# Performance work log

Hardware: AMD Instinct MI355X
Metric: run time of the kernel (lower is better)

The kernel has to match this reference:

```python
import jax, jax.numpy as jnp
import numpy as np

N = 10000
E = 160000
NEG_SLOPE = 0.2  # PyG GATConv default leaky_relu slope


def _gat_layer(x, src, dst, W, a_src, a_dst, b):
    """PyG GATConv with concat=True, add_self_loops=False.
    x: [N, Fin], W: [Fin, H*C], a_src/a_dst: [H, C], b: [H*C].
    """
    H, C = a_src.shape
    h = (x @ W).reshape(-1, H, C)                      # [N, H, C]
    al_s = jnp.sum(h * a_src, axis=-1)                 # [N, H]
    al_d = jnp.sum(h * a_dst, axis=-1)                 # [N, H]
    e = jax.nn.leaky_relu(al_s[src] + al_d[dst], NEG_SLOPE)  # [E, H]
    # segment softmax over edges grouped by destination node
    m = jax.ops.segment_max(e, dst, num_segments=N)    # [N, H]
    m = jnp.where(jnp.isfinite(m), m, 0.0)
    ex = jnp.exp(e - m[dst])                           # [E, H]
    den = jax.ops.segment_sum(ex, dst, num_segments=N)  # [N, H]
    alpha = ex / jnp.maximum(den[dst], 1e-16)          # [E, H]
    # scatter-add weighted source features
    out = jax.ops.segment_sum(alpha[:, :, None] * h[src], dst, num_segments=N)  # [N, H, C]
    return out.reshape(-1, H * C) + b


def setup_inputs() -> dict:
    key = jax.random.key(0)
    ks = jax.random.split(key, 16)
    s = 0.05
    return {
        "x": jax.random.normal(ks[0], (N, 300), jnp.float32),
        "edge_index": jax.random.randint(ks[1], (2, E), 0, N, jnp.int32),
        "W1": jax.random.normal(ks[2], (300, 512), jnp.float32) * s,
        "att_src1": jax.random.normal(ks[3], (4, 128), jnp.float32) * s,
        "att_dst1": jax.random.normal(ks[4], (4, 128), jnp.float32) * s,
        "b1": jax.random.normal(ks[5], (512,), jnp.float32) * s,
        "Wl1": jax.random.normal(ks[6], (300, 512), jnp.float32) * s,
        "bl1": jax.random.normal(ks[7], (512,), jnp.float32) * s,
        "W2": jax.random.normal(ks[8], (512, 2048), jnp.float32) * s,
        "att_src2": jax.random.normal(ks[9], (4, 512), jnp.float32) * s,
        "att_dst2": jax.random.normal(ks[10], (4, 512), jnp.float32) * s,
        "b2": jax.random.normal(ks[11], (2048,), jnp.float32) * s,
        "Wl2": jax.random.normal(ks[12], (512, 2048), jnp.float32) * s,
        "bl2": jax.random.normal(ks[13], (2048,), jnp.float32) * s,
    }


def reference(x, edge_index, W1, att_src1, att_dst1, b1, Wl1, bl1,
              W2, att_src2, att_dst2, b2, Wl2, bl2):
    src, dst = edge_index[0], edge_index[1]
    h1 = _gat_layer(x, src, dst, W1, att_src1, att_dst1, b1) + (x @ Wl1 + bl1)
    h1 = jax.nn.relu(h1)
    out = _gat_layer(h1, src, dst, W2, att_src2, att_dst2, b2) + (h1 @ Wl2 + bl2)
    return out
```

## Files before the change

kernel.cpp:

```cpp
#include <hip/hip_runtime.h>
#include <hip/hip_bf16.h>
#include <cstdint>


__device__ __forceinline__ float lrelu(float v) { return v >= 0.f ? v : 0.2f * v; }

__device__ __forceinline__ short f2bf(float x) {
  unsigned u = __float_as_uint(x);
  unsigned r = (u + 0x7fffu + ((u >> 16) & 1u)) >> 16;
  return (short)r;
}
__device__ __forceinline__ float bf2f(short b) {
  return __uint_as_float(((unsigned)(unsigned short)b) << 16);
}

typedef __attribute__((ext_vector_type(8))) short bf16x8;
typedef __attribute__((ext_vector_type(4))) float f32x4;

__device__ __forceinline__ void gload_lds16(const void* g, void* l) {
  auto gp = (const __attribute__((address_space(1))) unsigned int*)(uintptr_t)g;
  auto lp = (__attribute__((address_space(3))) unsigned int*)(uintptr_t)l;
  __builtin_amdgcn_global_load_lds(gp, lp, 16, 0, 0);
}

__global__ void count_edges_k(const int* __restrict__ dstv, int* __restrict__ counts, int E) {
  int e = blockIdx.x * 256 + threadIdx.x;
  if (e < E) atomicAdd(&counts[dstv[e]], 1);
}

__global__ void scan_k(const int* __restrict__ counts, int* __restrict__ rowptr,
                       int* __restrict__ cursor, int n) {
  __shared__ int wsum[16];
  __shared__ int s_base;
  int tid = threadIdx.x, lane = tid & 63, wv = tid >> 6;
  if (tid == 0) s_base = 0;
  __syncthreads();
  for (int base = 0; base < n; base += 1024) {
    int i = base + tid;
    int v = (i < n) ? counts[i] : 0;
    int x = v;
#pragma unroll
    for (int off = 1; off < 64; off <<= 1) {
      int t = __shfl_up(x, off);
      if (lane >= off) x += t;
    }
    if (lane == 63) wsum[wv] = x;
    __syncthreads();
    int woff = 0, tot = 0;
#pragma unroll
    for (int w = 0; w < 16; ++w) {
      int s = wsum[w];
      tot += s;
      if (w < wv) woff += s;
    }
    int b = s_base;
    if (i < n) {
      int excl = b + woff + x - v;
      rowptr[i] = excl;
      cursor[i] = excl;
    }
    __syncthreads();
    if (tid == 0) s_base = b + tot;
  }
  __syncthreads();
  if (tid == 0) rowptr[n] = s_base;
}

__global__ void fill_csr_k(const int* __restrict__ srcv, const int* __restrict__ dstv,
                           int* __restrict__ cursor, int* __restrict__ csr_src, int E) {
  int e = blockIdx.x * 256 + threadIdx.x;
  if (e < E) {
    int p = atomicAdd(&cursor[dstv[e]], 1);
    csr_src[p] = srcv[e];
  }
}

template <bool BIAS>
__global__ __launch_bounds__(256) void gemm_k(
    const float* __restrict__ A, const float* __restrict__ B,
    const float* __restrict__ bias, float* __restrict__ C,
    int M, int N, int K) {
  constexpr int BK = 16;
  __shared__ float As[BK][68];
  __shared__ float Bs[BK][64];
  int tid = threadIdx.x;
  int tx = tid & 15, ty = tid >> 4;
  int m0 = blockIdx.y * 64, n0 = blockIdx.x * 64;
  float acc[4][4] = {};
  int arow = tid >> 2, akq = (tid & 3) * 4;
  int bk = tid >> 4, bnq = (tid & 15) * 4;

  for (int k0 = 0; k0 < K; k0 += BK) {
    float4 av;
    int gm = m0 + arow, gk = k0 + akq;
    if (gm < M && gk + 3 < K) {
      av = *(const float4*)(A + (size_t)gm * K + gk);
    } else {
      av.x = (gm < M && gk + 0 < K) ? A[(size_t)gm * K + gk + 0] : 0.f;
      av.y = (gm < M && gk + 1 < K) ? A[(size_t)gm * K + gk + 1] : 0.f;
      av.z = (gm < M && gk + 2 < K) ? A[(size_t)gm * K + gk + 2] : 0.f;
      av.w = (gm < M && gk + 3 < K) ? A[(size_t)gm * K + gk + 3] : 0.f;
    }
    float4 bv = make_float4(0.f, 0.f, 0.f, 0.f);
    int gbk = k0 + bk;
    if (gbk < K) bv = *(const float4*)(B + (size_t)gbk * N + n0 + bnq);

    As[akq + 0][arow] = av.x;
    As[akq + 1][arow] = av.y;
    As[akq + 2][arow] = av.z;
    As[akq + 3][arow] = av.w;
    *(float4*)&Bs[bk][bnq] = bv;
    __syncthreads();

#pragma unroll
    for (int kk = 0; kk < BK; ++kk) {
      float4 a4 = *(const float4*)&As[kk][ty * 4];
      float4 b4 = *(const float4*)&Bs[kk][tx * 4];
      float a[4] = {a4.x, a4.y, a4.z, a4.w};
      float b[4] = {b4.x, b4.y, b4.z, b4.w};
#pragma unroll
      for (int i = 0; i < 4; ++i)
#pragma unroll
        for (int j = 0; j < 4; ++j) acc[i][j] = fmaf(a[i], b[j], acc[i][j]);
    }
    __syncthreads();
  }

#pragma unroll
  for (int i = 0; i < 4; ++i) {
    int gm = m0 + ty * 4 + i;
    if (gm >= M) continue;
    float4 o;
    float bx = 0.f, by = 0.f, bz = 0.f, bw = 0.f;
    if (BIAS) {
      bx = bias[n0 + tx * 4 + 0];
      by = bias[n0 + tx * 4 + 1];
      bz = bias[n0 + tx * 4 + 2];
      bw = bias[n0 + tx * 4 + 3];
    }
    o.x = acc[i][0] + bx;
    o.y = acc[i][1] + by;
    o.z = acc[i][2] + bz;
    o.w = acc[i][3] + bw;
    *(float4*)(C + (size_t)gm * N + n0 + tx * 4) = o;
  }
}

__global__ void wsplit_t_k(const float* __restrict__ W, short* __restrict__ Wth,
                           short* __restrict__ Wtl, int Nn) {
  int idx = blockIdx.x * 256 + threadIdx.x;
  if (idx >= Nn * 512) return;
  int k = idx & 511;
  int n = idx >> 9;
  float a = W[(size_t)k * Nn + n];
  short h = f2bf(a);
  Wth[idx] = h;
  Wtl[idx] = f2bf(a - bf2f(h));
}

template <bool BIAS>
__global__ __launch_bounds__(256) void gemm_bf16x3_k(
    const short* __restrict__ Ah, const short* __restrict__ Al,
    const short* __restrict__ Bh, const short* __restrict__ Bl,
    const float* __restrict__ bias, float* __restrict__ C,
    int M, int Nn, int K) {
  __shared__ __align__(16) short Ash[128 * 32];
  __shared__ __align__(16) short Asl[128 * 32];
  __shared__ __align__(16) short Bsh[128 * 32];
  __shared__ __align__(16) short Bsl[128 * 32];
  int tid = threadIdx.x, w = tid >> 6, l = tid & 63;
  int m0 = blockIdx.y * 128, n0 = blockIdx.x * 128;
  int wm = (w >> 1) * 64, wn = (w & 1) * 64;

  f32x4 acc[4][4] = {};

  int r_in = l >> 2;
  int kq = (l & 3) * 8;
  int arow_base = m0 + w * 32 + r_in;
  int brow_base = n0 + w * 32 + r_in;
  int lbase = (w * 32) * 32;

  int fr = l & 15, fk = (l >> 4) * 8;

  for (int k0 = 0; k0 < K; k0 += 32) {
    __syncthreads();
#pragma unroll
    for (int i = 0; i < 2; ++i) {
      int am = min(arow_base + i * 16, M - 1);
      int bn = brow_base + i * 16;
      size_t aoff = (size_t)am * K + k0 + kq;
      size_t boff = (size_t)bn * K + k0 + kq;
      int lofs = lbase + i * (16 * 32);
      gload_lds16(Ah + aoff, &Ash[lofs]);
      gload_lds16(Al + aoff, &Asl[lofs]);
      gload_lds16(Bh + boff, &Bsh[lofs]);
      gload_lds16(Bl + boff, &Bsl[lofs]);
    }
    __syncthreads();

    bf16x8 afh[4], afl[4], bfh[4], bfl[4];
#pragma unroll
    for (int t = 0; t < 4; ++t) {
      int ar = wm + t * 16 + fr;
      afh[t] = *(const bf16x8*)&Ash[ar * 32 + fk];
      afl[t] = *(const bf16x8*)&Asl[ar * 32 + fk];
      int br = wn + t * 16 + fr;
      bfh[t] = *(const bf16x8*)&Bsh[br * 32 + fk];
      bfl[t] = *(const bf16x8*)&Bsl[br * 32 + fk];
    }
#pragma unroll
    for (int mi = 0; mi < 4; ++mi)
#pragma unroll
      for (int ni = 0; ni < 4; ++ni) {
        acc[mi][ni] = __builtin_amdgcn_mfma_f32_16x16x32_bf16(afh[mi], bfh[ni], acc[mi][ni], 0, 0, 0);
        acc[mi][ni] = __builtin_amdgcn_mfma_f32_16x16x32_bf16(afh[mi], bfl[ni], acc[mi][ni], 0, 0, 0);
        acc[mi][ni] = __builtin_amdgcn_mfma_f32_16x16x32_bf16(afl[mi], bfh[ni], acc[mi][ni], 0, 0, 0);
      }
  }

  int fq = (l >> 4) * 4;
#pragma unroll
  for (int ni = 0; ni < 4; ++ni) {
    int gc = n0 + wn + ni * 16 + fr;
    float bv = BIAS ? bias[gc] : 0.f;
#pragma unroll
    for (int mi = 0; mi < 4; ++mi) {
      int grb = m0 + wm + mi * 16 + fq;
#pragma unroll
      for (int r = 0; r < 4; ++r) {
        int gr = grb + r;
        if (gr < M) C[(size_t)gr * Nn + gc] = acc[mi][ni][r] + bv;
      }
    }
  }
}

template <int C>
__global__ __launch_bounds__(256) void att_coef_k(
    const float* __restrict__ hfeat, const float* __restrict__ a_src,
    const float* __restrict__ a_dst, float* __restrict__ al_s,
    float* __restrict__ al_d, int n) {
  int wave = threadIdx.x >> 6, lane = threadIdx.x & 63;
  int node = blockIdx.x * 4 + wave;
  if (node >= n) return;
  constexpr int F = 4 * C;
  const float* hrow = hfeat + (size_t)node * F;
  float s[4] = {0, 0, 0, 0}, d[4] = {0, 0, 0, 0};
  for (int f = lane; f < F; f += 64) {
    float hv = hrow[f];
    int h = f / C;
    s[h] = fmaf(hv, a_src[f], s[h]);
    d[h] = fmaf(hv, a_dst[f], d[h]);
  }
#pragma unroll
  for (int off = 32; off; off >>= 1) {
#pragma unroll
    for (int h = 0; h < 4; ++h) {
      s[h] += __shfl_xor(s[h], off);
      d[h] += __shfl_xor(d[h], off);
    }
  }
  if (lane == 0) {
#pragma unroll
    for (int h = 0; h < 4; ++h) {
      al_s[node * 4 + h] = s[h];
      al_d[node * 4 + h] = d[h];
    }
  }
}

template <int F, int C, bool RELU, bool SPLIT>
__global__ __launch_bounds__(256) void gat_aggregate_k(
    const float* __restrict__ hfeat, const float* __restrict__ al_s,
    const float* __restrict__ al_d, const int* __restrict__ rowptr,
    const int* __restrict__ csr_src, const float* __restrict__ bias,
    const float* __restrict__ skip, float* __restrict__ out,
    short* __restrict__ oh, short* __restrict__ ol) {
  constexpr int NF = F / 256;
  int n = blockIdx.x;
  int tid = threadIdx.x;
  int lane = tid & 63, wave = tid >> 6;
  int r0 = rowptr[n], r1 = rowptr[n + 1];

  float ald[4];
#pragma unroll
  for (int h = 0; h < 4; ++h) ald[h] = al_d[n * 4 + h];

  __shared__ float red[4][4];
  __shared__ int src_sh[64];
  __shared__ float w_sh[64][4];

  float m[4] = {-3.4e38f, -3.4e38f, -3.4e38f, -3.4e38f};
  for (int e = r0 + tid; e < r1; e += 256) {
    int s = csr_src[e];
#pragma unroll
    for (int h = 0; h < 4; ++h) m[h] = fmaxf(m[h], lrelu(al_s[s * 4 + h] + ald[h]));
  }
#pragma unroll
  for (int off = 32; off; off >>= 1)
#pragma unroll
    for (int h = 0; h < 4; ++h) m[h] = fmaxf(m[h], __shfl_xor(m[h], off));
  if (lane == 0)
#pragma unroll
    for (int h = 0; h < 4; ++h) red[wave][h] = m[h];
  __syncthreads();
#pragma unroll
  for (int h = 0; h < 4; ++h)
    m[h] = fmaxf(fmaxf(red[0][h], red[1][h]), fmaxf(red[2][h], red[3][h]));
  __syncthreads();

  float den[4] = {0, 0, 0, 0};
  for (int e = r0 + tid; e < r1; e += 256) {
    int s = csr_src[e];
#pragma unroll
    for (int h = 0; h < 4; ++h) den[h] += expf(lrelu(al_s[s * 4 + h] + ald[h]) - m[h]);
  }
#pragma unroll
  for (int off = 32; off; off >>= 1)
#pragma unroll
    for (int h = 0; h < 4; ++h) den[h] += __shfl_xor(den[h], off);
  if (lane == 0)
#pragma unroll
    for (int h = 0; h < 4; ++h) red[wave][h] = den[h];
  __syncthreads();
  float rden[4];
#pragma unroll
  for (int h = 0; h < 4; ++h) {
    float dsum = red[0][h] + red[1][h] + red[2][h] + red[3][h];
    rden[h] = 1.f / fmaxf(dsum, 1e-16f);
  }

  float acc[NF] = {};
  for (int cs = r0; cs < r1; cs += 64) {
    int ce = min(64, r1 - cs);
    __syncthreads();
    if (tid < ce) src_sh[tid] = csr_src[cs + tid];
    if (tid < ce * 4) {
      int j = tid >> 2, h = tid & 3;
      int s = csr_src[cs + j];
      w_sh[j][h] = expf(lrelu(al_s[s * 4 + h] + ald[h]) - m[h]) * rden[h];
    }
    __syncthreads();
    for (int j = 0; j < ce; ++j) {
      int s = src_sh[j];
      const float* hrow = hfeat + (size_t)s * F;
#pragma unroll
      for (int i = 0; i < NF; ++i) {
        int f = tid + i * 256;
        acc[i] = fmaf(w_sh[j][f / C], hrow[f], acc[i]);
      }
    }
  }

  size_t rowoff = (size_t)n * F;
#pragma unroll
  for (int i = 0; i < NF; ++i) {
    int f = tid + i * 256;
    float v = acc[i] + bias[f] + skip[rowoff + f];
    if (RELU) v = fmaxf(v, 0.f);
    if (SPLIT) {
      short h = f2bf(v);
      oh[rowoff + f] = h;
      ol[rowoff + f] = f2bf(v - bf2f(h));
    } else {
      out[rowoff + f] = v;
    }
  }
}

extern "C" void kernel_launch(void* const* d_in, const int* in_sizes, int n_in,
                              void* d_out, int out_size, void* d_ws, size_t ws_size,
                              hipStream_t stream) {
  (void)n_in; (void)out_size; (void)ws_size;
  const float* x   = (const float*)d_in[0];
  const int*   ei  = (const int*)d_in[1];
  const float* W1  = (const float*)d_in[2];
  const float* as1 = (const float*)d_in[3];
  const float* ad1 = (const float*)d_in[4];
  const float* b1  = (const float*)d_in[5];
  const float* Wl1 = (const float*)d_in[6];
  const float* bl1 = (const float*)d_in[7];
  const float* W2  = (const float*)d_in[8];
  const float* as2 = (const float*)d_in[9];
  const float* ad2 = (const float*)d_in[10];
  const float* b2  = (const float*)d_in[11];
  const float* Wl2 = (const float*)d_in[12];
  const float* bl2 = (const float*)d_in[13];

  const int N = 10000;
  const int E = in_sizes[1] / 2;
  const int* srcv = ei;
  const int* dstv = ei + E;

  char* p = (char*)d_ws;
  float* hfeat = (float*)p; p += (size_t)N * 2048 * 4;
  float* s1 = hfeat + (size_t)N * 512;
  short* h1h = (short*)p; p += (size_t)N * 512 * 2;
  short* h1l = (short*)p; p += (size_t)N * 512 * 2;
  short* w2ht = (short*)p; p += (size_t)2048 * 512 * 2;
  short* w2lt = (short*)p; p += (size_t)2048 * 512 * 2;
  short* wl2ht = (short*)p; p += (size_t)2048 * 512 * 2;
  short* wl2lt = (short*)p; p += (size_t)2048 * 512 * 2;
  float* als = (float*)p; p += (size_t)N * 4 * 4;
  float* ald = (float*)p; p += (size_t)N * 4 * 4;
  int* rowptr = (int*)p; p += (N + 1) * 4;
  int* cursor = (int*)p; p += N * 4;
  int* counts = (int*)p; p += N * 4;
  int* csr_src = (int*)p; p += (size_t)E * 4;

  hipMemsetAsync(counts, 0, N * sizeof(int), stream);
  count_edges_k<<<(E + 255) / 256, 256, 0, stream>>>(dstv, counts, E);
  scan_k<<<1, 1024, 0, stream>>>(counts, rowptr, cursor, N);
  fill_csr_k<<<(E + 255) / 256, 256, 0, stream>>>(srcv, dstv, cursor, csr_src, E);

  wsplit_t_k<<<(2048 * 512 + 255) / 256, 256, 0, stream>>>(W2, w2ht, w2lt, 2048);
  wsplit_t_k<<<(2048 * 512 + 255) / 256, 256, 0, stream>>>(Wl2, wl2ht, wl2lt, 2048);

  gemm_k<false><<<dim3(8, (N + 63) / 64), 256, 0, stream>>>(x, W1, nullptr, hfeat, N, 512, 300);
  gemm_k<true><<<dim3(8, (N + 63) / 64), 256, 0, stream>>>(x, Wl1, bl1, s1, N, 512, 300);
  att_coef_k<128><<<(N + 3) / 4, 256, 0, stream>>>(hfeat, as1, ad1, als, ald, N);
  gat_aggregate_k<512, 128, true, true><<<N, 256, 0, stream>>>(
      hfeat, als, ald, rowptr, csr_src, b1, s1, nullptr, h1h, h1l);

  gemm_bf16x3_k<false><<<dim3(2048 / 128, (N + 127) / 128), 256, 0, stream>>>(
      h1h, h1l, w2ht, w2lt, nullptr, hfeat, N, 2048, 512);
  gemm_bf16x3_k<true><<<dim3(2048 / 128, (N + 127) / 128), 256, 0, stream>>>(
      h1h, h1l, wl2ht, wl2lt, bl2, (float*)d_out, N, 2048, 512);
  att_coef_k<512><<<(N + 3) / 4, 256, 0, stream>>>(hfeat, as2, ad2, als, ald, N);
  gat_aggregate_k<2048, 512, false, false><<<N, 256, 0, stream>>>(
      hfeat, als, ald, rowptr, csr_src, b2, (float*)d_out, (float*)d_out, nullptr, nullptr);
}
```

Measured before the change: 722.7 us.

## Use split-bf16 MFMA GEMM for layer 1 and split softmax from SpMM aggregation

Replaces the fp32 SIMT GEMM for the first layer with the split-bf16 (hi/lo) MFMA GEMM, padding K from 300 to 320 and adding conversion kernels for x, W1 and Wl1. It also splits the fused per-node aggregation into an edge-softmax kernel that writes per-edge alpha to a workspace and a wave-per-node, column-tiled SpMM kernel with two accumulators. The goal is to use matrix cores for layer 1 and to get more parallelism and less block-level synchronisation in the aggregation. In exchange it adds extra conversion passes, an alpha buffer round-trip through memory, and repeated reads of csr_src and alpha across column tiles.

```diff
diff --git a/kernel.cpp b/kernel.cpp
--- a/kernel.cpp
+++ b/kernel.cpp
@@ -75,84 +75,23 @@
   }
 }
 
-template <bool BIAS>
-__global__ __launch_bounds__(256) void gemm_k(
-    const float* __restrict__ A, const float* __restrict__ B,
-    const float* __restrict__ bias, float* __restrict__ C,
-    int M, int N, int K) {
-  constexpr int BK = 16;
-  __shared__ float As[BK][68];
-  __shared__ float Bs[BK][64];
-  int tid = threadIdx.x;
-  int tx = tid & 15, ty = tid >> 4;
-  int m0 = blockIdx.y * 64, n0 = blockIdx.x * 64;
-  float acc[4][4] = {};
-  int arow = tid >> 2, akq = (tid & 3) * 4;
-  int bk = tid >> 4, bnq = (tid & 15) * 4;
-
-  for (int k0 = 0; k0 < K; k0 += BK) {
-    float4 av;
-    int gm = m0 + arow, gk = k0 + akq;
-    if (gm < M && gk + 3 < K) {
-      av = *(const float4*)(A + (size_t)gm * K + gk);
-    } else {
-      av.x = (gm < M && gk + 0 < K) ? A[(size_t)gm * K + gk + 0] : 0.f;
-      av.y = (gm < M && gk + 1 < K) ? A[(size_t)gm * K + gk + 1] : 0.f;
-      av.z = (gm < M && gk + 2 < K) ? A[(size_t)gm * K + gk + 2] : 0.f;
-      av.w = (gm < M && gk + 3 < K) ? A[(size_t)gm * K + gk + 3] : 0.f;
-    }
-    float4 bv = make_float4(0.f, 0.f, 0.f, 0.f);
-    int gbk = k0 + bk;
-    if (gbk < K) bv = *(const float4*)(B + (size_t)gbk * N + n0 + bnq);
-
-    As[akq + 0][arow] = av.x;
-    As[akq + 1][arow] = av.y;
-    As[akq + 2][arow] = av.z;
-    As[akq + 3][arow] = av.w;
-    *(float4*)&Bs[bk][bnq] = bv;
-    __syncthreads();
-
-#pragma unroll
-    for (int kk = 0; kk < BK; ++kk) {
-      float4 a4 = *(const float4*)&As[kk][ty * 4];
-      float4 b4 = *(const float4*)&Bs[kk][tx * 4];
-      float a[4] = {a4.x, a4.y, a4.z, a4.w};
-      float b[4] = {b4.x, b4.y, b4.z, b4.w};
-#pragma unroll
-      for (int i = 0; i < 4; ++i)
-#pragma unroll
-        for (int j = 0; j < 4; ++j) acc[i][j] = fmaf(a[i], b[j], acc[i][j]);
-    }
-    __syncthreads();
-  }
-
-#pragma unroll
-  for (int i = 0; i < 4; ++i) {
-    int gm = m0 + ty * 4 + i;
-    if (gm >= M) continue;
-    float4 o;
-    float bx = 0.f, by = 0.f, bz = 0.f, bw = 0.f;
-    if (BIAS) {
-      bx = bias[n0 + tx * 4 + 0];
-      by = bias[n0 + tx * 4 + 1];
-      bz = bias[n0 + tx * 4 + 2];
-      bw = bias[n0 + tx * 4 + 3];
-    }
-    o.x = acc[i][0] + bx;
-    o.y = acc[i][1] + by;
-    o.z = acc[i][2] + bz;
-    o.w = acc[i][3] + bw;
-    *(float4*)(C + (size_t)gm * N + n0 + tx * 4) = o;
-  }
+__global__ void xsplit_k(const float* __restrict__ x, short* __restrict__ xh,
+                         short* __restrict__ xl, int total) {
+  int idx = blockIdx.x * 256 + threadIdx.x;
+  if (idx >= total) return;
+  int n = idx / 320, k = idx - n * 320;
+  float v = (k < 300) ? x[(size_t)n * 300 + k] : 0.f;
+  short h = f2bf(v);
+  xh[idx] = h;
+  xl[idx] = f2bf(v - bf2f(h));
 }
 
 __global__ void wsplit_t_k(const float* __restrict__ W, short* __restrict__ Wth,
-                           short* __restrict__ Wtl, int Nn) {
+                           short* __restrict__ Wtl, int Nn, int Kin, int Kpad) {
   int idx = blockIdx.x * 256 + threadIdx.x;
-  if (idx >= Nn * 512) return;
-  int k = idx & 511;
-  int n = idx >> 9;
-  float a = W[(size_t)k * Nn + n];
+  if (idx >= Nn * Kpad) return;
+  int n = idx / Kpad, k = idx - n * Kpad;
+  float a = (k < Kin) ? W[(size_t)k * Nn + n] : 0.f;
   short h = f2bf(a);
   Wth[idx] = h;
   Wtl[idx] = f2bf(a - bf2f(h));
@@ -269,102 +208,87 @@
   }
 }
 
+__global__ __launch_bounds__(256) void edge_alpha_k(
+    const float* __restrict__ al_s, const float* __restrict__ al_d,
+    const int* __restrict__ rowptr, const int* __restrict__ csr_src,
+    float* __restrict__ alpha, int N) {
+  int wave = threadIdx.x >> 6, lane = threadIdx.x & 63;
+  int n = blockIdx.x * 4 + wave;
+  if (n >= N) return;
+  int r0 = rowptr[n], r1 = rowptr[n + 1];
+  float ald[4];
+#pragma unroll
+  for (int h = 0; h < 4; ++h) ald[h] = al_d[n * 4 + h];
+
+  float m[4] = {-3.4e38f, -3.4e38f, -3.4e38f, -3.4e38f};
+  for (int e = r0 + lane; e < r1; e += 64) {
+    int s = csr_src[e];
+#pragma unroll
+    for (int h = 0; h < 4; ++h) m[h] = fmaxf(m[h], lrelu(al_s[s * 4 + h] + ald[h]));
+  }
+#pragma unroll
+  for (int off = 32; off; off >>= 1)
+#pragma unroll
+    for (int h = 0; h < 4; ++h) m[h] = fmaxf(m[h], __shfl_xor(m[h], off));
+
+  float den[4] = {0, 0, 0, 0};
+  for (int e = r0 + lane; e < r1; e += 64) {
+    int s = csr_src[e];
+#pragma unroll
+    for (int h = 0; h < 4; ++h) den[h] += expf(lrelu(al_s[s * 4 + h] + ald[h]) - m[h]);
+  }
+#pragma unroll
+  for (int off = 32; off; off >>= 1)
+#pragma unroll
+    for (int h = 0; h < 4; ++h) den[h] += __shfl_xor(den[h], off);
+
+  float rden[4];
+#pragma unroll
+  for (int h = 0; h < 4; ++h) rden[h] = 1.f / fmaxf(den[h], 1e-16f);
+
+  for (int e = r0 + lane; e < r1; e += 64) {
+    int s = csr_src[e];
+#pragma unroll
+    for (int h = 0; h < 4; ++h)
+      alpha[(size_t)e * 4 + h] = expf(lrelu(al_s[s * 4 + h] + ald[h]) - m[h]) * rden[h];
+  }
+}
+
 template <int F, int C, bool RELU, bool SPLIT>
-__global__ __launch_bounds__(256) void gat_aggregate_k(
-    const float* __restrict__ hfeat, const float* __restrict__ al_s,
-    const float* __restrict__ al_d, const int* __restrict__ rowptr,
-    const int* __restrict__ csr_src, const float* __restrict__ bias,
-    const float* __restrict__ skip, float* __restrict__ out,
-    short* __restrict__ oh, short* __restrict__ ol) {
-  constexpr int NF = F / 256;
-  int n = blockIdx.x;
-  int tid = threadIdx.x;
-  int lane = tid & 63, wave = tid >> 6;
+__global__ __launch_bounds__(256) void spmm_k(
+    const float* __restrict__ hfeat, const float* __restrict__ alpha,
+    const int* __restrict__ rowptr, const int* __restrict__ csr_src,
+    const float* __restrict__ bias, const float* __restrict__ skip,
+    float* __restrict__ out, short* __restrict__ oh, short* __restrict__ ol, int N) {
+  int wave = threadIdx.x >> 6, lane = threadIdx.x & 63;
+  int n = blockIdx.x * 4 + wave;
+  if (n >= N) return;
+  int col = blockIdx.y * 64 + lane;
+  int head = (blockIdx.y * 64) / C;
   int r0 = rowptr[n], r1 = rowptr[n + 1];
 
-  float ald[4];
-#pragma unroll
-  for (int h = 0; h < 4; ++h) ald[h] = al_d[n * 4 + h];
-
-  __shared__ float red[4][4];
-  __shared__ int src_sh[64];
-  __shared__ float w_sh[64][4];
-
-  float m[4] = {-3.4e38f, -3.4e38f, -3.4e38f, -3.4e38f};
-  for (int e = r0 + tid; e < r1; e += 256) {
-    int s = csr_src[e];
-#pragma unroll
-    for (int h = 0; h < 4; ++h) m[h] = fmaxf(m[h], lrelu(al_s[s * 4 + h] + ald[h]));
-  }
-#pragma unroll
-  for (int off = 32; off; off >>= 1)
-#pragma unroll
-    for (int h = 0; h < 4; ++h) m[h] = fmaxf(m[h], __shfl_xor(m[h], off));
-  if (lane == 0)
-#pragma unroll
-    for (int h = 0; h < 4; ++h) red[wave][h] = m[h];
-  __syncthreads();
-#pragma unroll
-  for (int h = 0; h < 4; ++h)
-    m[h] = fmaxf(fmaxf(red[0][h], red[1][h]), fmaxf(red[2][h], red[3][h]));
-  __syncthreads();
-
-  float den[4] = {0, 0, 0, 0};
-  for (int e = r0 + tid; e < r1; e += 256) {
-    int s = csr_src[e];
-#pragma unroll
-    for (int h = 0; h < 4; ++h) den[h] += expf(lrelu(al_s[s * 4 + h] + ald[h]) - m[h]);
-  }
-#pragma unroll
-  for (int off = 32; off; off >>= 1)
-#pragma unroll
-    for (int h = 0; h < 4; ++h) den[h] += __shfl_xor(den[h], off);
-  if (lane == 0)
-#pragma unroll
-    for (int h = 0; h < 4; ++h) red[wave][h] = den[h];
-  __syncthreads();
-  float rden[4];
-#pragma unroll
-  for (int h = 0; h < 4; ++h) {
-    float dsum = red[0][h] + red[1][h] + red[2][h] + red[3][h];
-    rden[h] = 1.f / fmaxf(dsum, 1e-16f);
-  }
-
-  float acc[NF] = {};
-  for (int cs = r0; cs < r1; cs += 64) {
-    int ce = min(64, r1 - cs);
-    __syncthreads();
-    if (tid < ce) src_sh[tid] = csr_src[cs + tid];
-    if (tid < ce * 4) {
-      int j = tid >> 2, h = tid & 3;
-      int s = csr_src[cs + j];
-      w_sh[j][h] = expf(lrelu(al_s[s * 4 + h] + ald[h]) - m[h]) * rden[h];
-    }
-    __syncthreads();
-    for (int j = 0; j < ce; ++j) {
-      int s = src_sh[j];
-      const float* hrow = hfeat + (size_t)s * F;
-#pragma unroll
-      for (int i = 0; i < NF; ++i) {
-        int f = tid + i * 256;
-        acc[i] = fmaf(w_sh[j][f / C], hrow[f], acc[i]);
-      }
-    }
-  }
-
-  size_t rowoff = (size_t)n * F;
-#pragma unroll
-  for (int i = 0; i < NF; ++i) {
-    int f = tid + i * 256;
-    float v = acc[i] + bias[f] + skip[rowoff + f];
-    if (RELU) v = fmaxf(v, 0.f);
-    if (SPLIT) {
-      short h = f2bf(v);
-      oh[rowoff + f] = h;
-      ol[rowoff + f] = f2bf(v - bf2f(h));
-    } else {
-      out[rowoff + f] = v;
-    }
+  float acc0 = 0.f, acc1 = 0.f;
+  int e = r0;
+  for (; e + 1 < r1; e += 2) {
+    int s0 = csr_src[e], s1 = csr_src[e + 1];
+    float a0 = alpha[(size_t)e * 4 + head];
+    float a1 = alpha[(size_t)(e + 1) * 4 + head];
+    acc0 = fmaf(a0, hfeat[(size_t)s0 * F + col], acc0);
+    acc1 = fmaf(a1, hfeat[(size_t)s1 * F + col], acc1);
+  }
+  if (e < r1) {
+    int s0 = csr_src[e];
+    float a0 = alpha[(size_t)e * 4 + head];
+    acc0 = fmaf(a0, hfeat[(size_t)s0 * F + col], acc0);
+  }
+  float v = acc0 + acc1 + bias[col] + skip[(size_t)n * F + col];
+  if (RELU) v = fmaxf(v, 0.f);
+  if (SPLIT) {
+    short h = f2bf(v);
+    oh[(size_t)n * F + col] = h;
+    ol[(size_t)n * F + col] = f2bf(v - bf2f(h));
+  } else {
+    out[(size_t)n * F + col] = v;
   }
 }
 
@@ -395,14 +319,21 @@
   char* p = (char*)d_ws;
   float* hfeat = (float*)p; p += (size_t)N * 2048 * 4;
   float* s1 = hfeat + (size_t)N * 512;
+  short* xh = (short*)(hfeat + (size_t)N * 1024);
+  short* xl = xh + (size_t)N * 320;
   short* h1h = (short*)p; p += (size_t)N * 512 * 2;
   short* h1l = (short*)p; p += (size_t)N * 512 * 2;
   short* w2ht = (short*)p; p += (size_t)2048 * 512 * 2;
   short* w2lt = (short*)p; p += (size_t)2048 * 512 * 2;
   short* wl2ht = (short*)p; p += (size_t)2048 * 512 * 2;
   short* wl2lt = (short*)p; p += (size_t)2048 * 512 * 2;
+  short* w1ht = (short*)p; p += (size_t)512 * 320 * 2;
+  short* w1lt = (short*)p; p += (size_t)512 * 320 * 2;
+  short* wl1ht = (short*)p; p += (size_t)512 * 320 * 2;
+  short* wl1lt = (short*)p; p += (size_t)512 * 320 * 2;
   float* als = (float*)p; p += (size_t)N * 4 * 4;
   float* ald = (float*)p; p += (size_t)N * 4 * 4;
+  float* alpha = (float*)p; p += (size_t)E * 4 * 4;
   int* rowptr = (int*)p; p += (N + 1) * 4;
   int* cursor = (int*)p; p += N * 4;
   int* counts = (int*)p; p += N * 4;
@@ -413,20 +344,27 @@
   scan_k<<<1, 1024, 0, stream>>>(counts, rowptr, cursor, N);
   fill_csr_k<<<(E + 255) / 256, 256, 0, stream>>>(srcv, dstv, cursor, csr_src, E);
 
-  wsplit_t_k<<<(2048 * 512 + 255) / 256, 256, 0, stream>>>(W2, w2ht, w2lt, 2048);
-  wsplit_t_k<<<(2048 * 512 + 255) / 256, 256, 0, stream>>>(Wl2, wl2ht, wl2lt, 2048);
-
-  gemm_k<false><<<dim3(8, (N + 63) / 64), 256, 0, stream>>>(x, W1, nullptr, hfeat, N, 512, 300);
-  gemm_k<true><<<dim3(8, (N + 63) / 64), 256, 0, stream>>>(x, Wl1, bl1, s1, N, 512, 300);
+  xsplit_k<<<(N * 320 + 255) / 256, 256, 0, stream>>>(x, xh, xl, N * 320);
+  wsplit_t_k<<<(512 * 320 + 255) / 256, 256, 0, stream>>>(W1, w1ht, w1lt, 512, 300, 320);
+  wsplit_t_k<<<(512 * 320 + 255) / 256, 256, 0, stream>>>(Wl1, wl1ht, wl1lt, 512, 300, 320);
+  wsplit_t_k<<<(2048 * 512 + 255) / 256, 256, 0, stream>>>(W2, w2ht, w2lt, 2048, 512, 512);
+  wsplit_t_k<<<(2048 * 512 + 255) / 256, 256, 0, stream>>>(Wl2, wl2ht, wl2lt, 2048, 512, 512);
+
+  gemm_bf16x3_k<false><<<dim3(512 / 128, (N + 127) / 128), 256, 0, stream>>>(
+      xh, xl, w1ht, w1lt, nullptr, hfeat, N, 512, 320);
+  gemm_bf16x3_k<true><<<dim3(512 / 128, (N + 127) / 128), 256, 0, stream>>>(
+      xh, xl, wl1ht, wl1lt, bl1, s1, N, 512, 320);
   att_coef_k<128><<<(N + 3) / 4, 256, 0, stream>>>(hfeat, as1, ad1, als, ald, N);
-  gat_aggregate_k<512, 128, true, true><<<N, 256, 0, stream>>>(
-      hfeat, als, ald, rowptr, csr_src, b1, s1, nullptr, h1h, h1l);
+  edge_alpha_k<<<(N + 3) / 4, 256, 0, stream>>>(als, ald, rowptr, csr_src, alpha, N);
+  spmm_k<512, 128, true, true><<<dim3((N + 3) / 4, 512 / 64), 256, 0, stream>>>(
+      hfeat, alpha, rowptr, csr_src, b1, s1, nullptr, h1h, h1l, N);
 
   gemm_bf16x3_k<false><<<dim3(2048 / 128, (N + 127) / 128), 256, 0, stream>>>(
       h1h, h1l, w2ht, w2lt, nullptr, hfeat, N, 2048, 512);
   gemm_bf16x3_k<true><<<dim3(2048 / 128, (N + 127) / 128), 256, 0, stream>>>(
       h1h, h1l, wl2ht, wl2lt, bl2, (float*)d_out, N, 2048, 512);
   att_coef_k<512><<<(N + 3) / 4, 256, 0, stream>>>(hfeat, as2, ad2, als, ald, N);
-  gat_aggregate_k<2048, 512, false, false><<<N, 256, 0, stream>>>(
-      hfeat, als, ald, rowptr, csr_src, b2, (float*)d_out, (float*)d_out, nullptr, nullptr);
-}
+  edge_alpha_k<<<(N + 3) / 4, 256, 0, stream>>>(als, ald, rowptr, csr_src, alpha, N);
+  spmm_k<2048, 512, false, false><<<dim3((N + 3) / 4, 2048 / 64), 256, 0, stream>>>(
+      hfeat, alpha, rowptr, csr_src, b2, (float*)d_out, (float*)d_out, nullptr, nullptr, N);
+}
```

Measured after the change: 799.6 us. 10.6% more time.
